# Kernel optimization log

Hardware: AMD Instinct MI355X
Metric: run time of the kernel (lower is better)

## Reference

```python
import jax, jax.numpy as jnp
import numpy as np

B, L, C, H, DK, MAXREL = 4, 1024, 768, 12, 64, 7
NEG = -2.0 ** 15  # masked_fill value


def _rel_pos_table(L, m):
    # abs distance, compressed logarithmically beyond m, clipped to [0, 2m]
    i = jnp.arange(L, dtype=jnp.float32)
    d = jnp.abs(i[:, None] - i[None, :])
    comp = m + jnp.log2(jnp.maximum(d - m, 1.0))
    d = jnp.where(d > m, comp, d)
    return jnp.clip(d, 0, 2 * m).astype(jnp.int32)  # [L, L]


def setup_inputs() -> dict:
    key = jax.random.key(0)
    ks = jax.random.split(key, 16)
    s = 0.02
    return {
        "qx": jax.random.normal(ks[0], (B, L, C), jnp.float32),
        "kx": jax.random.normal(ks[1], (B, L, C), jnp.float32),
        "vx": jax.random.normal(ks[2], (B, L, C), jnp.float32),
        "WQ_w": jax.random.normal(ks[3], (C, H * DK), jnp.float32) * s,
        "WQ_b": jnp.zeros((H * DK,), jnp.float32),
        "WK_w": jax.random.normal(ks[4], (C, H * DK), jnp.float32) * s,
        "WK_b": jnp.zeros((H * DK,), jnp.float32),
        "WV_w": jax.random.normal(ks[5], (C, H * DK), jnp.float32) * s,
        "WV_b": jnp.zeros((H * DK,), jnp.float32),
        "WO_w": jax.random.normal(ks[6], (H * DK, C), jnp.float32) * s,
        "WO_b": jnp.zeros((C,), jnp.float32),
        "embK": jax.random.normal(ks[7], (2 * MAXREL + 1, H), jnp.float32),
        "embB": jax.random.normal(ks[8], (2 * MAXREL + 1, H), jnp.float32) * s,
        "preScores": jax.random.normal(ks[9], (B, H, L, L), jnp.float32) * 0.1,
        "maskPAD": jnp.ones((B, L, L), jnp.int32),
    }


def reference(qx, kx, vx, WQ_w, WQ_b, WK_w, WK_b, WV_w, WV_b, WO_w, WO_b,
              embK, embB, preScores, maskPAD):
    q = (qx @ WQ_w + WQ_b).reshape(B, L, H, DK).transpose(0, 2, 1, 3)  # [B,H,L,dk]
    k = (kx @ WK_w + WK_b).reshape(B, L, H, DK).transpose(0, 2, 1, 3)
    v = (vx @ WV_w + WV_b).reshape(B, L, H, DK).transpose(0, 2, 1, 3)

    scores = jnp.einsum('bhid,bhjd->bhij', q, k) / np.sqrt(DK).astype(np.float32)

    tab = _rel_pos_table(L, MAXREL)                 # [L, L] int
    relK = jnp.transpose(embK[tab], (2, 1, 0))      # [H, L, L] (torch transpose(0,-1))
    relB = jnp.transpose(embB[tab], (2, 1, 0))
    scores = scores * relK[None] + relB[None]

    scores = scores + preScores
    scores = jnp.where((maskPAD == 0)[:, None, :, :], jnp.float32(NEG), scores)

    alpha = jax.nn.softmax(scores, axis=-1)         # dropout is identity in eval
    z = jnp.einsum('bhij,bhjd->bhid', alpha, v)     # [B,H,L,dk]
    z = z.transpose(0, 2, 1, 3).reshape(B, L, H * DK)
    z = z @ WO_w + WO_b
    return (z, scores)
```

## Files before the change

### kernel.cpp

```cpp
#include <hip/hip_runtime.h>
#include <stdint.h>


typedef __attribute__((ext_vector_type(4))) float f32x4;
typedef __attribute__((ext_vector_type(4))) int   i32x4;
typedef __attribute__((ext_vector_type(8))) short short8;
typedef __attribute__((ext_vector_type(4))) unsigned int u32x4;
typedef __attribute__((ext_vector_type(2))) unsigned int u32x2;

__device__ __forceinline__ unsigned short f2bf(float f) {
  unsigned int u = __float_as_uint(f);
  u += 0x7fffu + ((u >> 16) & 1u);
  return (unsigned short)(u >> 16);
}

__global__ __launch_bounds__(256) void conv_x_kernel(
    const float* __restrict__ qx, const float* __restrict__ kx,
    const float* __restrict__ vx, unsigned short* __restrict__ out) {
  int v = blockIdx.x * 256 + threadIdx.x;
  int mat = v / 786432;
  int r = v - mat * 786432;
  const float* src = (mat == 0) ? qx : (mat == 1) ? kx : vx;
  f32x4 x = ((const f32x4*)src)[r];
  union { unsigned short s[4]; u32x2 u; } o;
  o.s[0] = f2bf(x[0]); o.s[1] = f2bf(x[1]); o.s[2] = f2bf(x[2]); o.s[3] = f2bf(x[3]);
  ((u32x2*)out)[v] = o.u;
}

__global__ __launch_bounds__(256) void conv_w_kernel(
    const float* __restrict__ w0, const float* __restrict__ w1,
    const float* __restrict__ w2, const float* __restrict__ w3,
    unsigned short* __restrict__ out) {
  __shared__ float T[64][65];
  int bx = blockIdx.x;
  int mat = bx / 144; int t2 = bx - mat * 144;
  int kt = t2 / 12, nt = t2 - kt * 12;
  int k0 = kt * 64, n0 = nt * 64;
  const float* W = (mat == 0) ? w0 : (mat == 1) ? w1 : (mat == 2) ? w2 : w3;
  unsigned short* WT = out + (size_t)mat * 589824;
  int t = threadIdx.x;
  int lr = t >> 4;
  int lc = (t & 15) * 4;
#pragma unroll
  for (int p = 0; p < 4; p++) {
    int row = p * 16 + lr;
    f32x4 x = *(const f32x4*)&W[(size_t)(k0 + row) * 768 + n0 + lc];
    T[lc + 0][row] = x[0]; T[lc + 1][row] = x[1];
    T[lc + 2][row] = x[2]; T[lc + 3][row] = x[3];
  }
  __syncthreads();
#pragma unroll
  for (int p = 0; p < 4; p++) {
    int row = p * 16 + lr;
    union { unsigned short s[4]; u32x2 u; } o;
    o.s[0] = f2bf(T[row][lc + 0]); o.s[1] = f2bf(T[row][lc + 1]);
    o.s[2] = f2bf(T[row][lc + 2]); o.s[3] = f2bf(T[row][lc + 3]);
    *(u32x2*)&WT[(size_t)(n0 + row) * 768 + k0 + lc] = o.u;
  }
}

__global__ __launch_bounds__(256, 2) void qkv_gemm_kernel(
    const unsigned short* __restrict__ xbf, const unsigned short* __restrict__ wt,
    const float* __restrict__ bq, const float* __restrict__ bk, const float* __restrict__ bv,
    unsigned short* __restrict__ qo, unsigned short* __restrict__ ko,
    unsigned short* __restrict__ vto) {
  __shared__ unsigned short SM[2][2][128 * 72];
  int bx = blockIdx.x;
  int mat = bx / 192; int rem = bx - mat * 192;
  int mt = rem / 6, nt = rem - mt * 6;
  int m0 = mt * 128, n0 = nt * 128;
  const unsigned short* A = xbf + (size_t)mat * 4096 * 768;
  const unsigned short* Bm = wt + (size_t)mat * 768 * 768;
  int t = threadIdx.x;
  int wave = t >> 6, lane = t & 63;
  int wm = (wave >> 1) * 64, wn = (wave & 1) * 64;
  int col = lane & 15, quad = lane >> 4;
  int srow = t >> 3;
  int sch = (t & 7) * 8;

  f32x4 acc[4][4];
#pragma unroll
  for (int i = 0; i < 4; i++)
#pragma unroll
    for (int j = 0; j < 4; j++) acc[i][j] = (f32x4){0.f, 0.f, 0.f, 0.f};

  u32x4 ra[4], rb[4];
#pragma unroll
  for (int p = 0; p < 4; p++) {
    ra[p] = *(const u32x4*)&A[(size_t)(m0 + srow + p * 32) * 768 + sch];
    rb[p] = *(const u32x4*)&Bm[(size_t)(n0 + srow + p * 32) * 768 + sch];
  }
#pragma unroll
  for (int p = 0; p < 4; p++) {
    *(u32x4*)&SM[0][0][(srow + p * 32) * 72 + sch] = ra[p];
    *(u32x4*)&SM[0][1][(srow + p * 32) * 72 + sch] = rb[p];
  }
#pragma unroll
  for (int p = 0; p < 4; p++) {
    ra[p] = *(const u32x4*)&A[(size_t)(m0 + srow + p * 32) * 768 + 64 + sch];
    rb[p] = *(const u32x4*)&Bm[(size_t)(n0 + srow + p * 32) * 768 + 64 + sch];
  }
  __syncthreads();

  for (int it = 0; it < 12; ++it) {
    const unsigned short* As = SM[it & 1][0];
    const unsigned short* Bs = SM[it & 1][1];
#pragma unroll
    for (int c = 0; c < 2; c++) {
      short8 af[4], bf[4];
#pragma unroll
      for (int i = 0; i < 4; i++) {
        af[i] = *(const short8*)&As[(wm + i * 16 + col) * 72 + c * 32 + quad * 8];
        bf[i] = *(const short8*)&Bs[(wn + i * 16 + col) * 72 + c * 32 + quad * 8];
      }
#pragma unroll
      for (int i = 0; i < 4; i++)
#pragma unroll
        for (int j = 0; j < 4; j++)
          acc[i][j] = __builtin_amdgcn_mfma_f32_16x16x32_bf16(af[i], bf[j], acc[i][j], 0, 0, 0);
    }
    if (it < 11) {
      unsigned short* An = SM[(it + 1) & 1][0];
      unsigned short* Bn = SM[(it + 1) & 1][1];
#pragma unroll
      for (int p = 0; p < 4; p++) {
        *(u32x4*)&An[(srow + p * 32) * 72 + sch] = ra[p];
        *(u32x4*)&Bn[(srow + p * 32) * 72 + sch] = rb[p];
      }
      if (it < 10) {
        int kk2 = (it + 2) * 64;
#pragma unroll
        for (int p = 0; p < 4; p++) {
          ra[p] = *(const u32x4*)&A[(size_t)(m0 + srow + p * 32) * 768 + kk2 + sch];
          rb[p] = *(const u32x4*)&Bm[(size_t)(n0 + srow + p * 32) * 768 + kk2 + sch];
        }
      }
      __syncthreads();
    }
  }

  if (mat != 2) {
    const float* bias = (mat == 0) ? bq : bk;
    unsigned short* dst = (mat == 0) ? qo : ko;
#pragma unroll
    for (int j = 0; j < 4; j++) {
      int gn = n0 + wn + j * 16 + col;
      float bsv = bias[gn];
      int h = gn >> 6, d = gn & 63;
#pragma unroll
      for (int i = 0; i < 4; i++) {
#pragma unroll
        for (int r = 0; r < 4; r++) {
          int gm = m0 + wm + i * 16 + quad * 4 + r;
          int b = gm >> 10, l = gm & 1023;
          dst[((size_t)(b * 12 + h) * 1024 + l) * 64 + d] = f2bf(acc[i][j][r] + bsv);
        }
      }
    }
  } else {
    unsigned short* Tr = &SM[0][0][0];
    __syncthreads();
#pragma unroll
    for (int j = 0; j < 4; j++) {
      int n = wn + j * 16 + col;
      float bsv = bv[n0 + n];
#pragma unroll
      for (int i = 0; i < 4; i++) {
        int m = wm + i * 16 + quad * 4;
        union { unsigned short s[4]; u32x2 u; } pk;
#pragma unroll
        for (int r = 0; r < 4; r++) pk.s[r] = f2bf(acc[i][j][r] + bsv);
        *(u32x2*)&Tr[(size_t)n * 132 + m] = pk.u;
      }
    }
    __syncthreads();
#pragma unroll
    for (int p = 0; p < 8; p++) {
      int row = (t >> 4) + p * 16;
      int ch = (t & 15) * 8;
      u32x4 val = *(const u32x4*)&Tr[(size_t)row * 132 + ch];
      int gn = n0 + row;
      int h = gn >> 6, d = gn & 63;
      int gm = m0 + ch;
      int b = gm >> 10, l = gm & 1023;
      *(u32x4*)&vto[((size_t)(b * 12 + h) * 64 + d) * 1024 + l] = val;
    }
  }
}

struct KV { u32x4 k0, k1, v0, v1; };

__device__ __forceinline__ void attn_body(
    int jt, const unsigned short* KsC, const unsigned short* VsC,
    unsigned short* KsN, unsigned short* VsN,
    f32x4* preC, f32x4* preN, KV& kvW, KV& kvF,
    const short8* qf, f32x4* oacc, float& m_s, float& l_s,
    const unsigned short* kbase, const unsigned short* vbase,
    const float* pbase, const int* mbase, float* sbase,
    unsigned short* Ps, const float* eK, const float* eB,
    int lrow, int gi, int srow, int sch, int col, int quad, int wave) {
  const int j0 = jt * 64;
  i32x4 mk[4];
#pragma unroll
  for (int ns = 0; ns < 4; ns++)
    mk[ns] = *(const i32x4*)&mbase[(size_t)lrow * 1024 + j0 + ns * 16 + quad * 4];
  if (jt < 15) {
    int jp1 = (jt + 1) * 64;
#pragma unroll
    for (int ns = 0; ns < 4; ns++)
      preN[ns] = *(const f32x4*)&pbase[(size_t)lrow * 1024 + jp1 + ns * 16 + quad * 4];
  }
  if (jt < 14) {
    int jp2 = (jt + 2) * 64;
    kvF.k0 = *(const u32x4*)&kbase[(size_t)(jp2 + srow) * 64 + sch];
    kvF.k1 = *(const u32x4*)&kbase[(size_t)(jp2 + srow + 32) * 64 + sch];
    kvF.v0 = *(const u32x4*)&vbase[(size_t)srow * 1024 + jp2 + sch];
    kvF.v1 = *(const u32x4*)&vbase[(size_t)(srow + 32) * 1024 + jp2 + sch];
  }
  f32x4 sacc[4];
#pragma unroll
  for (int ns = 0; ns < 4; ns++) sacc[ns] = (f32x4){0.f, 0.f, 0.f, 0.f};
#pragma unroll
  for (int c = 0; c < 2; c++) {
#pragma unroll
    for (int ns = 0; ns < 4; ns++) {
      short8 kf = *(const short8*)&KsC[(ns * 16 + col) * 72 + c * 32 + quad * 8];
      sacc[ns] = __builtin_amdgcn_mfma_f32_16x16x32_bf16(kf, qf[c], sacc[ns], 0, 0, 0);
    }
  }
  float sv[4][4];
#pragma unroll
  for (int ns = 0; ns < 4; ns++) {
    int gj0 = j0 + ns * 16 + quad * 4;
    f32x4 sout;
#pragma unroll
    for (int r = 0; r < 4; r++) {
      int dd = gi - (gj0 + r); dd = dd < 0 ? -dd : dd;
      int idx;
      if (dd <= 7) idx = dd;
      else { idx = 38 - __clz(dd - 7); idx = idx > 14 ? 14 : idx; }
      float s = sacc[ns][r] * 0.125f * eK[idx] + eB[idx] + preC[ns][r];
      if (mk[ns][r] == 0) s = -32768.0f;
      sout[r] = s; sv[ns][r] = s;
    }
    *(f32x4*)&sbase[(size_t)lrow * 1024 + gj0] = sout;
  }
  float mx = sv[0][0];
#pragma unroll
  for (int ns = 0; ns < 4; ns++)
#pragma unroll
    for (int r = 0; r < 4; r++) mx = fmaxf(mx, sv[ns][r]);
  mx = fmaxf(mx, __shfl_xor(mx, 16));
  mx = fmaxf(mx, __shfl_xor(mx, 32));
  float mn = fmaxf(m_s, mx);
  float alpha = __expf(m_s - mn);
  float rs = 0.f;
#pragma unroll
  for (int ns = 0; ns < 4; ns++)
#pragma unroll
    for (int r = 0; r < 4; r++) { float p = __expf(sv[ns][r] - mn); sv[ns][r] = p; rs += p; }
  rs += __shfl_xor(rs, 16); rs += __shfl_xor(rs, 32);
  l_s = l_s * alpha + rs;
  m_s = mn;
#pragma unroll
  for (int nd = 0; nd < 4; nd++)
#pragma unroll
    for (int r = 0; r < 4; r++) oacc[nd][r] *= alpha;
#pragma unroll
  for (int ns = 0; ns < 4; ns++) {
    union { unsigned short s[4]; u32x2 u; } pk;
#pragma unroll
    for (int r = 0; r < 4; r++) pk.s[r] = f2bf(sv[ns][r]);
    *(u32x2*)&Ps[(size_t)lrow * 72 + ns * 16 + quad * 4] = pk.u;
  }
#pragma unroll
  for (int c2 = 0; c2 < 2; c2++) {
    short8 pf = *(const short8*)&Ps[(wave * 16 + col) * 72 + c2 * 32 + quad * 8];
#pragma unroll
    for (int nd = 0; nd < 4; nd++) {
      short8 vf = *(const short8*)&VsC[(nd * 16 + col) * 72 + c2 * 32 + quad * 8];
      oacc[nd] = __builtin_amdgcn_mfma_f32_16x16x32_bf16(vf, pf, oacc[nd], 0, 0, 0);
    }
  }
  if (jt < 15) {
    *(u32x4*)&KsN[srow * 72 + sch] = kvW.k0;
    *(u32x4*)&KsN[(srow + 32) * 72 + sch] = kvW.k1;
    *(u32x4*)&VsN[srow * 72 + sch] = kvW.v0;
    *(u32x4*)&VsN[(srow + 32) * 72 + sch] = kvW.v1;
    __syncthreads();
  }
}

__global__ __launch_bounds__(256, 3) void attn_kernel(
    const unsigned short* __restrict__ q, const unsigned short* __restrict__ k,
    const unsigned short* __restrict__ vt, const float* __restrict__ preS,
    const int* __restrict__ maskP, const float* __restrict__ embK,
    const float* __restrict__ embB, float* __restrict__ scores,
    unsigned short* __restrict__ zpre) {
  __shared__ unsigned short Qs[64 * 72];
  __shared__ unsigned short KsB[2][64 * 72];
  __shared__ unsigned short VsB[2][64 * 72];
  __shared__ float eKs[16], eBs[16];
  int bx = blockIdx.x;
  int slice = bx % 48, it = bx / 48;
  int b = slice / 12, h = slice - b * 12;
  int i0 = it * 64;
  int t = threadIdx.x, wave = t >> 6, lane = t & 63;
  int col = lane & 15, quad = lane >> 4;
  int srow = t >> 3, sch = (t & 7) * 8;

  if (t < 15) { eKs[t] = embK[t * 12 + h]; eBs[t] = embB[t * 12 + h]; }

  const unsigned short* qbase = q + ((size_t)(b * 12 + h) * 1024 + i0) * 64;
  const unsigned short* kbase = k + (size_t)(b * 12 + h) * 1024 * 64;
  const unsigned short* vbase = vt + (size_t)(b * 12 + h) * 64 * 1024;
  const float* pbase = preS + ((size_t)(b * 12 + h) * 1024 + i0) * 1024;
  const int* mbase = maskP + ((size_t)b * 1024 + i0) * 1024;
  float* sbase = scores + ((size_t)(b * 12 + h) * 1024 + i0) * 1024;
  int lrow = wave * 16 + col;
  int gi = i0 + lrow;

#pragma unroll
  for (int p = 0; p < 2; p++) {
    int row = srow + p * 32;
    *(u32x4*)&Qs[row * 72 + sch] = *(const u32x4*)&qbase[(size_t)row * 64 + sch];
  }
  __syncthreads();
  short8 qf[2];
  qf[0] = *(const short8*)&Qs[(wave * 16 + col) * 72 + quad * 8];
  qf[1] = *(const short8*)&Qs[(wave * 16 + col) * 72 + 32 + quad * 8];

  f32x4 oacc[4];
#pragma unroll
  for (int nd = 0; nd < 4; nd++) oacc[nd] = (f32x4){0.f, 0.f, 0.f, 0.f};
  float m_s = -3.0e38f, l_s = 0.f;

  KV kvA, kvB;
  f32x4 preA[4], preB[4];
  kvA.k0 = *(const u32x4*)&kbase[(size_t)srow * 64 + sch];
  kvA.k1 = *(const u32x4*)&kbase[(size_t)(srow + 32) * 64 + sch];
  kvA.v0 = *(const u32x4*)&vbase[(size_t)srow * 1024 + sch];
  kvA.v1 = *(const u32x4*)&vbase[(size_t)(srow + 32) * 1024 + sch];
  *(u32x4*)&KsB[0][srow * 72 + sch] = kvA.k0;
  *(u32x4*)&KsB[0][(srow + 32) * 72 + sch] = kvA.k1;
  *(u32x4*)&VsB[0][srow * 72 + sch] = kvA.v0;
  *(u32x4*)&VsB[0][(srow + 32) * 72 + sch] = kvA.v1;
#pragma unroll
  for (int ns = 0; ns < 4; ns++)
    preA[ns] = *(const f32x4*)&pbase[(size_t)lrow * 1024 + ns * 16 + quad * 4];
  kvB.k0 = *(const u32x4*)&kbase[(size_t)(64 + srow) * 64 + sch];
  kvB.k1 = *(const u32x4*)&kbase[(size_t)(64 + srow + 32) * 64 + sch];
  kvB.v0 = *(const u32x4*)&vbase[(size_t)srow * 1024 + 64 + sch];
  kvB.v1 = *(const u32x4*)&vbase[(size_t)(srow + 32) * 1024 + 64 + sch];
  __syncthreads();

  unsigned short* Ps = Qs;
  for (int jt = 0; jt < 16; jt += 2) {
    attn_body(jt,     KsB[0], VsB[0], KsB[1], VsB[1], preA, preB, kvB, kvA,
              qf, oacc, m_s, l_s, kbase, vbase, pbase, mbase, sbase,
              Ps, eKs, eBs, lrow, gi, srow, sch, col, quad, wave);
    attn_body(jt + 1, KsB[1], VsB[1], KsB[0], VsB[0], preB, preA, kvA, kvB,
              qf, oacc, m_s, l_s, kbase, vbase, pbase, mbase, sbase,
              Ps, eKs, eBs, lrow, gi, srow, sch, col, quad, wave);
  }

  float inv = 1.0f / fmaxf(l_s, 1e-30f);
  unsigned short* zb = zpre + ((size_t)(b * 12 + h) * 1024 + i0 + lrow) * 64;
#pragma unroll
  for (int nd = 0; nd < 4; nd++) {
    union { unsigned short s[4]; u32x2 u; } zk;
#pragma unroll
    for (int r = 0; r < 4; r++) zk.s[r] = f2bf(oacc[nd][r] * inv);
    *(u32x2*)&zb[nd * 16 + quad * 4] = zk.u;
  }
}

__global__ __launch_bounds__(256, 3) void out_gemm_kernel(
    const unsigned short* __restrict__ zpre, const unsigned short* __restrict__ wot,
    const float* __restrict__ wob, float* __restrict__ zout) {
  __shared__ unsigned short SM[2][2][64 * 72];
  int bx = blockIdx.x;
  int mt = bx / 12, nt = bx - mt * 12;
  int m0 = mt * 64, n0 = nt * 64;
  int t = threadIdx.x;
  int wave = t >> 6, lane = t & 63;
  int wm = (wave >> 1) * 32, wn = (wave & 1) * 32;
  int col = lane & 15, quad = lane >> 4;
  int srow = t >> 3, sch = (t & 7) * 8;
  int gmA0 = m0 + srow, gmA1 = m0 + srow + 32;
  int bA0 = gmA0 >> 10, lA0 = gmA0 & 1023;
  int bA1 = gmA1 >> 10, lA1 = gmA1 & 1023;

  f32x4 acc[2][2];
#pragma unroll
  for (int i = 0; i < 2; i++)
#pragma unroll
    for (int j = 0; j < 2; j++) acc[i][j] = (f32x4){0.f, 0.f, 0.f, 0.f};

  u32x4 ra[2], rb[2];
  ra[0] = *(const u32x4*)&zpre[((size_t)(bA0 * 12 + 0) * 1024 + lA0) * 64 + sch];
  ra[1] = *(const u32x4*)&zpre[((size_t)(bA1 * 12 + 0) * 1024 + lA1) * 64 + sch];
  rb[0] = *(const u32x4*)&wot[(size_t)(n0 + srow) * 768 + sch];
  rb[1] = *(const u32x4*)&wot[(size_t)(n0 + srow + 32) * 768 + sch];
  *(u32x4*)&SM[0][0][srow * 72 + sch] = ra[0];
  *(u32x4*)&SM[0][0][(srow + 32) * 72 + sch] = ra[1];
  *(u32x4*)&SM[0][1][srow * 72 + sch] = rb[0];
  *(u32x4*)&SM[0][1][(srow + 32) * 72 + sch] = rb[1];
  ra[0] = *(const u32x4*)&zpre[((size_t)(bA0 * 12 + 1) * 1024 + lA0) * 64 + sch];
  ra[1] = *(const u32x4*)&zpre[((size_t)(bA1 * 12 + 1) * 1024 + lA1) * 64 + sch];
  rb[0] = *(const u32x4*)&wot[(size_t)(n0 + srow) * 768 + 64 + sch];
  rb[1] = *(const u32x4*)&wot[(size_t)(n0 + srow + 32) * 768 + 64 + sch];
  __syncthreads();

  for (int it = 0; it < 12; ++it) {
    const unsigned short* As = SM[it & 1][0];
    const unsigned short* Bs = SM[it & 1][1];
#pragma unroll
    for (int c = 0; c < 2; c++) {
      short8 af[2], bf[2];
#pragma unroll
      for (int i = 0; i < 2; i++) {
        af[i] = *(const short8*)&As[(wm + i * 16 + col) * 72 + c * 32 + quad * 8];
        bf[i] = *(const short8*)&Bs[(wn + i * 16 + col) * 72 + c * 32 + quad * 8];
      }
#pragma unroll
      for (int i = 0; i < 2; i++)
#pragma unroll
        for (int j = 0; j < 2; j++)
          acc[i][j] = __builtin_amdgcn_mfma_f32_16x16x32_bf16(af[i], bf[j], acc[i][j], 0, 0, 0);
    }
    if (it < 11) {
      unsigned short* An = SM[(it + 1) & 1][0];
      unsigned short* Bn = SM[(it + 1) & 1][1];
      *(u32x4*)&An[srow * 72 + sch] = ra[0];
      *(u32x4*)&An[(srow + 32) * 72 + sch] = ra[1];
      *(u32x4*)&Bn[srow * 72 + sch] = rb[0];
      *(u32x4*)&Bn[(srow + 32) * 72 + sch] = rb[1];
      if (it < 10) {
        int hh = it + 2;
        ra[0] = *(const u32x4*)&zpre[((size_t)(bA0 * 12 + hh) * 1024 + lA0) * 64 + sch];
        ra[1] = *(const u32x4*)&zpre[((size_t)(bA1 * 12 + hh) * 1024 + lA1) * 64 + sch];
        rb[0] = *(const u32x4*)&wot[(size_t)(n0 + srow) * 768 + hh * 64 + sch];
        rb[1] = *(const u32x4*)&wot[(size_t)(n0 + srow + 32) * 768 + hh * 64 + sch];
      }
      __syncthreads();
    }
  }
#pragma unroll
  for (int j = 0; j < 2; j++) {
    int gn = n0 + wn + j * 16 + col;
    float bsv = wob[gn];
#pragma unroll
    for (int i = 0; i < 2; i++) {
#pragma unroll
      for (int r = 0; r < 4; r++) {
        int gm = m0 + wm + i * 16 + quad * 4 + r;
        zout[(size_t)gm * 768 + gn] = acc[i][j][r] + bsv;
      }
    }
  }
}

extern "C" void kernel_launch(void* const* d_in, const int* in_sizes, int n_in,
                              void* d_out, int out_size, void* d_ws, size_t ws_size,
                              hipStream_t stream) {
  const float* qx   = (const float*)d_in[0];
  const float* kx   = (const float*)d_in[1];
  const float* vx   = (const float*)d_in[2];
  const float* WQ_w = (const float*)d_in[3];
  const float* WQ_b = (const float*)d_in[4];
  const float* WK_w = (const float*)d_in[5];
  const float* WK_b = (const float*)d_in[6];
  const float* WV_w = (const float*)d_in[7];
  const float* WV_b = (const float*)d_in[8];
  const float* WO_w = (const float*)d_in[9];
  const float* WO_b = (const float*)d_in[10];
  const float* embK = (const float*)d_in[11];
  const float* embB = (const float*)d_in[12];
  const float* preS = (const float*)d_in[13];
  const int* maskP  = (const int*)d_in[14];

  float* zout = (float*)d_out;
  float* scores = zout + 3145728;
  unsigned short* xbf = (unsigned short*)scores;

  char* ws = (char*)d_ws;
  unsigned short* wt  = (unsigned short*)(ws);
  unsigned short* qb  = (unsigned short*)(ws + 4718592);
  unsigned short* kb  = (unsigned short*)(ws + 11010048);
  unsigned short* vtb = (unsigned short*)(ws + 17301504);
  unsigned short* zp  = (unsigned short*)(ws + 23592960);

  conv_x_kernel<<<9216, 256, 0, stream>>>(qx, kx, vx, xbf);
  conv_w_kernel<<<576, 256, 0, stream>>>(WQ_w, WK_w, WV_w, WO_w, wt);
  qkv_gemm_kernel<<<576, 256, 0, stream>>>(xbf, wt, WQ_b, WK_b, WV_b, qb, kb, vtb);
  attn_kernel<<<768, 256, 0, stream>>>(qb, kb, vtb, preS, maskP, embK, embB, scores, zp);
  out_gemm_kernel<<<192 * 4, 256, 0, stream>>>(zp, wt + 3 * 589824, WO_b, zout);
}
```

Before: 492.0 us.

## Stagger attention key-tile start per block, prefetch mask, use nontemporal score I/O

Each attention block now begins its key/value sweep at a tile offset derived from its query tile index and wraps around. This spreads concurrent blocks across different K/V and preScores columns, which should reduce contention on the same memory regions. The mask tile is now prefetched one iteration ahead alongside preScores instead of being loaded synchronously. PreScores loads and score stores use nontemporal hints to avoid polluting cache with streaming data. The extra double-buffered mask registers may raise register pressure under the 3-blocks-per-SM launch bound.

New measurement: 504.9 us. 1.03x slower.

```diff
diff --git a/kernel.cpp b/kernel.cpp
--- a/kernel.cpp
+++ b/kernel.cpp
@@ -191,31 +191,28 @@
 struct KV { u32x4 k0, k1, v0, v1; };
 
 __device__ __forceinline__ void attn_body(
-    int jt, const unsigned short* KsC, const unsigned short* VsC,
+    int j0, int j1, int j2, bool pf1, bool pf2,
+    const unsigned short* KsC, const unsigned short* VsC,
     unsigned short* KsN, unsigned short* VsN,
-    f32x4* preC, f32x4* preN, KV& kvW, KV& kvF,
+    f32x4* preC, f32x4* preN, i32x4* mkC, i32x4* mkN, KV& kvW, KV& kvF,
     const short8* qf, f32x4* oacc, float& m_s, float& l_s,
     const unsigned short* kbase, const unsigned short* vbase,
     const float* pbase, const int* mbase, float* sbase,
     unsigned short* Ps, const float* eK, const float* eB,
     int lrow, int gi, int srow, int sch, int col, int quad, int wave) {
-  const int j0 = jt * 64;
-  i32x4 mk[4];
-#pragma unroll
-  for (int ns = 0; ns < 4; ns++)
-    mk[ns] = *(const i32x4*)&mbase[(size_t)lrow * 1024 + j0 + ns * 16 + quad * 4];
-  if (jt < 15) {
-    int jp1 = (jt + 1) * 64;
-#pragma unroll
-    for (int ns = 0; ns < 4; ns++)
-      preN[ns] = *(const f32x4*)&pbase[(size_t)lrow * 1024 + jp1 + ns * 16 + quad * 4];
-  }
-  if (jt < 14) {
-    int jp2 = (jt + 2) * 64;
-    kvF.k0 = *(const u32x4*)&kbase[(size_t)(jp2 + srow) * 64 + sch];
-    kvF.k1 = *(const u32x4*)&kbase[(size_t)(jp2 + srow + 32) * 64 + sch];
-    kvF.v0 = *(const u32x4*)&vbase[(size_t)srow * 1024 + jp2 + sch];
-    kvF.v1 = *(const u32x4*)&vbase[(size_t)(srow + 32) * 1024 + jp2 + sch];
+  if (pf1) {
+#pragma unroll
+    for (int ns = 0; ns < 4; ns++) {
+      preN[ns] = __builtin_nontemporal_load(
+          (const f32x4*)&pbase[(size_t)lrow * 1024 + j1 + ns * 16 + quad * 4]);
+      mkN[ns] = *(const i32x4*)&mbase[(size_t)lrow * 1024 + j1 + ns * 16 + quad * 4];
+    }
+  }
+  if (pf2) {
+    kvF.k0 = *(const u32x4*)&kbase[(size_t)(j2 + srow) * 64 + sch];
+    kvF.k1 = *(const u32x4*)&kbase[(size_t)(j2 + srow + 32) * 64 + sch];
+    kvF.v0 = *(const u32x4*)&vbase[(size_t)srow * 1024 + j2 + sch];
+    kvF.v1 = *(const u32x4*)&vbase[(size_t)(srow + 32) * 1024 + j2 + sch];
   }
   f32x4 sacc[4];
 #pragma unroll
@@ -240,10 +237,10 @@
       if (dd <= 7) idx = dd;
       else { idx = 38 - __clz(dd - 7); idx = idx > 14 ? 14 : idx; }
       float s = sacc[ns][r] * 0.125f * eK[idx] + eB[idx] + preC[ns][r];
-      if (mk[ns][r] == 0) s = -32768.0f;
+      if (mkC[ns][r] == 0) s = -32768.0f;
       sout[r] = s; sv[ns][r] = s;
     }
-    *(f32x4*)&sbase[(size_t)lrow * 1024 + gj0] = sout;
+    __builtin_nontemporal_store(sout, (f32x4*)&sbase[(size_t)lrow * 1024 + gj0]);
   }
   float mx = sv[0][0];
 #pragma unroll
@@ -282,7 +279,7 @@
       oacc[nd] = __builtin_amdgcn_mfma_f32_16x16x32_bf16(vf, pf, oacc[nd], 0, 0, 0);
     }
   }
-  if (jt < 15) {
+  if (pf1) {
     *(u32x4*)&KsN[srow * 72 + sch] = kvW.k0;
     *(u32x4*)&KsN[(srow + 32) * 72 + sch] = kvW.k1;
     *(u32x4*)&VsN[srow * 72 + sch] = kvW.v0;
@@ -335,31 +332,45 @@
   for (int nd = 0; nd < 4; nd++) oacc[nd] = (f32x4){0.f, 0.f, 0.f, 0.f};
   float m_s = -3.0e38f, l_s = 0.f;
 
+  int jt0 = it & 15;
+  int t0 = jt0 * 64;
+  int t1 = ((jt0 + 1) & 15) * 64;
+
   KV kvA, kvB;
   f32x4 preA[4], preB[4];
-  kvA.k0 = *(const u32x4*)&kbase[(size_t)srow * 64 + sch];
-  kvA.k1 = *(const u32x4*)&kbase[(size_t)(srow + 32) * 64 + sch];
-  kvA.v0 = *(const u32x4*)&vbase[(size_t)srow * 1024 + sch];
-  kvA.v1 = *(const u32x4*)&vbase[(size_t)(srow + 32) * 1024 + sch];
+  i32x4 mkA[4], mkB[4];
+  kvA.k0 = *(const u32x4*)&kbase[(size_t)(t0 + srow) * 64 + sch];
+  kvA.k1 = *(const u32x4*)&kbase[(size_t)(t0 + srow + 32) * 64 + sch];
+  kvA.v0 = *(const u32x4*)&vbase[(size_t)srow * 1024 + t0 + sch];
+  kvA.v1 = *(const u32x4*)&vbase[(size_t)(srow + 32) * 1024 + t0 + sch];
   *(u32x4*)&KsB[0][srow * 72 + sch] = kvA.k0;
   *(u32x4*)&KsB[0][(srow + 32) * 72 + sch] = kvA.k1;
   *(u32x4*)&VsB[0][srow * 72 + sch] = kvA.v0;
   *(u32x4*)&VsB[0][(srow + 32) * 72 + sch] = kvA.v1;
 #pragma unroll
-  for (int ns = 0; ns < 4; ns++)
-    preA[ns] = *(const f32x4*)&pbase[(size_t)lrow * 1024 + ns * 16 + quad * 4];
-  kvB.k0 = *(const u32x4*)&kbase[(size_t)(64 + srow) * 64 + sch];
-  kvB.k1 = *(const u32x4*)&kbase[(size_t)(64 + srow + 32) * 64 + sch];
-  kvB.v0 = *(const u32x4*)&vbase[(size_t)srow * 1024 + 64 + sch];
-  kvB.v1 = *(const u32x4*)&vbase[(size_t)(srow + 32) * 1024 + 64 + sch];
+  for (int ns = 0; ns < 4; ns++) {
+    preA[ns] = __builtin_nontemporal_load(
+        (const f32x4*)&pbase[(size_t)lrow * 1024 + t0 + ns * 16 + quad * 4]);
+    mkA[ns] = *(const i32x4*)&mbase[(size_t)lrow * 1024 + t0 + ns * 16 + quad * 4];
+  }
+  kvB.k0 = *(const u32x4*)&kbase[(size_t)(t1 + srow) * 64 + sch];
+  kvB.k1 = *(const u32x4*)&kbase[(size_t)(t1 + srow + 32) * 64 + sch];
+  kvB.v0 = *(const u32x4*)&vbase[(size_t)srow * 1024 + t1 + sch];
+  kvB.v1 = *(const u32x4*)&vbase[(size_t)(srow + 32) * 1024 + t1 + sch];
   __syncthreads();
 
   unsigned short* Ps = Qs;
-  for (int jt = 0; jt < 16; jt += 2) {
-    attn_body(jt,     KsB[0], VsB[0], KsB[1], VsB[1], preA, preB, kvB, kvA,
+  for (int n = 0; n < 16; n += 2) {
+    int ja = ((jt0 + n) & 15) * 64;
+    int jb = ((jt0 + n + 1) & 15) * 64;
+    int jc = ((jt0 + n + 2) & 15) * 64;
+    int jd = ((jt0 + n + 3) & 15) * 64;
+    attn_body(ja, jb, jc, (n) < 15, (n) < 14,
+              KsB[0], VsB[0], KsB[1], VsB[1], preA, preB, mkA, mkB, kvB, kvA,
               qf, oacc, m_s, l_s, kbase, vbase, pbase, mbase, sbase,
               Ps, eKs, eBs, lrow, gi, srow, sch, col, quad, wave);
-    attn_body(jt + 1, KsB[1], VsB[1], KsB[0], VsB[0], preB, preA, kvA, kvB,
+    attn_body(jb, jc, jd, (n + 1) < 15, (n + 1) < 14,
+              KsB[1], VsB[1], KsB[0], VsB[0], preB, preA, mkB, mkA, kvA, kvB,
               qf, oacc, m_s, l_s, kbase, vbase, pbase, mbase, sbase,
               Ps, eKs, eBs, lrow, gi, srow, sch, col, quad, wave);
   }
```
